# Optimization experiments

Hardware: AMD Instinct MI355X
Metric: run time of the kernel (lower is better)

The kernel has to match this reference:

```python
import jax, jax.numpy as jnp
import numpy as np

DIM = 768
NUM_HEADS = 12
HEAD_DIM = DIM // NUM_HEADS
SCALE = HEAD_DIM ** -0.5
NEG = -9e15


def setup_inputs() -> dict:
    key = jax.random.key(0)
    ks = jax.random.split(key, 8)
    B, N, M, C = 4, 1024, 2048, DIM
    q = jax.random.normal(ks[0], (B, N, C), dtype=jnp.float32)
    kv = jax.random.normal(ks[1], (B, M, C), dtype=jnp.float32)
    mask = jax.random.randint(ks[2], (B, 1, N, M), 0, 2, dtype=jnp.int32)
    s = 1.0 / np.sqrt(C)
    Wq = jax.random.normal(ks[3], (C, C), dtype=jnp.float32) * s      # nn.Linear(dim, dim), no bias
    Wkv = jax.random.normal(ks[4], (2 * C, C), dtype=jnp.float32) * s  # nn.Linear(dim, 2*dim), no bias
    Wproj = jax.random.normal(ks[5], (C, C), dtype=jnp.float32) * s
    bproj = jax.random.normal(ks[6], (C,), dtype=jnp.float32) * s
    return {"q": q, "kv": kv, "Wq": Wq, "Wkv": Wkv, "Wproj": Wproj, "bproj": bproj, "mask": mask}


def reference(q, kv, Wq, Wkv, Wproj, bproj, mask):
    B, M, C = kv.shape
    _, N, _ = q.shape
    H, d = NUM_HEADS, HEAD_DIM
    # kv projection -> [B, M, 2, H, d] -> k, v: [B, H, M, d]
    kvp = (kv @ Wkv.T).reshape(B, M, 2, H, d)
    k = kvp[:, :, 0].transpose(0, 2, 1, 3)
    v = kvp[:, :, 1].transpose(0, 2, 1, 3)
    # q projection -> [B, H, N, d], pre-scaled
    qp = (q @ Wq.T).reshape(B, N, H, d).transpose(0, 2, 1, 3) * SCALE
    attn = jnp.einsum('bhnd,bhmd->bhnm', qp, k)  # [B, H, N, M]
    attn = jnp.where(mask == 0, NEG, attn)
    attn = jax.nn.softmax(attn, axis=-1)
    # attn_drop / proj_drop have rate 0.0 (eval): identity
    x = jnp.einsum('bhnm,bhmd->bhnd', attn, v)
    x = x.transpose(0, 2, 1, 3).reshape(B, N, C)
    x = x @ Wproj.T + bproj
    return x
```

## Files before the change

### kernel.cpp

```cpp
#include <hip/hip_runtime.h>
#include <hip/hip_bf16.h>


typedef short    s16x8  __attribute__((ext_vector_type(8)));
typedef short    s16x4  __attribute__((ext_vector_type(4)));
typedef float    f32x4  __attribute__((ext_vector_type(4)));
typedef _Float16 f16x8  __attribute__((ext_vector_type(8)));
typedef _Float16 f16x4  __attribute__((ext_vector_type(4)));
typedef _Float16 f16x2  __attribute__((ext_vector_type(2)));

#define NUM_H 12
#define DIM   768
#define NQ    1024
#define MK    2048
#define QK_SCALE_LOG2E 0.18033688f

__device__ __forceinline__ short f2h(float v) {
    _Float16 h = (_Float16)v;
    return __builtin_bit_cast(short, h);
}
__device__ __forceinline__ float h2f(short v) {
    return (float)__builtin_bit_cast(_Float16, v);
}
__device__ __forceinline__ f32x4 mfma16x32(f16x8 a, f16x8 b, f32x4 c) {
    return __builtin_amdgcn_mfma_f32_16x16x32_f16(a, b, c, 0, 0, 0);
}
__device__ __forceinline__ f16x2 pk2h(float a, float b) {
    return __builtin_bit_cast(f16x2, __builtin_amdgcn_cvt_pkrtz(a, b));
}

__global__ __launch_bounds__(256) void prep_kernel(
    const float* __restrict__ q, const float* __restrict__ kv,
    const float* __restrict__ Wq, const float* __restrict__ Wkv,
    const float* __restrict__ Wp, const int* __restrict__ mask,
    short* __restrict__ q_h, short* __restrict__ kv_h,
    short* __restrict__ Wq_h, short* __restrict__ Wkv_h,
    short* __restrict__ Wp_h, unsigned char* __restrict__ mbytes)
{
    int bid = blockIdx.x;
    if (bid < 5760) {
        const float* s; short* d; long base;
        if (bid < 1536)      { s = q;   d = q_h;   base = (long)bid * 2048; }
        else if (bid < 4608) { s = kv;  d = kv_h;  base = (long)(bid - 1536) * 2048; }
        else if (bid < 4896) { s = Wq;  d = Wq_h;  base = (long)(bid - 4608) * 2048; }
        else if (bid < 5472) { s = Wkv; d = Wkv_h; base = (long)(bid - 4896) * 2048; }
        else                 { s = Wp;  d = Wp_h;  base = (long)(bid - 5472) * 2048; }
        long i = base + threadIdx.x * 8;
        float4 a = *(const float4*)(s + i);
        float4 b = *(const float4*)(s + i + 4);
        s16x8 r;
        r[0] = f2h(a.x); r[1] = f2h(a.y); r[2] = f2h(a.z); r[3] = f2h(a.w);
        r[4] = f2h(b.x); r[5] = f2h(b.y); r[6] = f2h(b.z); r[7] = f2h(b.w);
        *(s16x8*)(d + i) = r;
    } else {
        long base = (long)(bid - 5760) * 2048 + threadIdx.x * 8;
        int4 m0 = *(const int4*)(mask + base);
        int4 m1 = *(const int4*)(mask + base + 4);
        unsigned v = (unsigned)(m0.x != 0)        | ((unsigned)(m0.y != 0) << 1)
                   | ((unsigned)(m0.z != 0) << 2) | ((unsigned)(m0.w != 0) << 3)
                   | ((unsigned)(m1.x != 0) << 4) | ((unsigned)(m1.y != 0) << 5)
                   | ((unsigned)(m1.z != 0) << 6) | ((unsigned)(m1.w << 7) & 0x80);
        v = (v & 0x7f) | ((unsigned)(m1.w != 0) << 7);
        mbytes[base >> 3] = (unsigned char)v;
    }
}

__device__ __forceinline__ void gemm_core(
    short* smem,
    const short* __restrict__ A, const short* __restrict__ Bt,
    int Ncols, int mode, const float* __restrict__ bias,
    short* __restrict__ outb, short* __restrict__ outb2,
    float* __restrict__ outf, int bid)
{
    short (*As)[72] = (short(*)[72])smem;
    short (*Bs)[72] = (short(*)[72])(smem + 9216);

    int ntiles = Ncols >> 7;
    int m0 = (bid / ntiles) << 7;
    int n0 = (bid % ntiles) << 7;
    int t = threadIdx.x;
    int w = t >> 6, lane = t & 63, quad = lane >> 4, l16 = lane & 15;
    int wm = (w & 1) << 6, wn = (w >> 1) << 6;

    f32x4 zero4 = {0.f, 0.f, 0.f, 0.f};
    f32x4 acc[4][4];
    for (int i = 0; i < 4; i++)
        for (int j = 0; j < 4; j++) acc[i][j] = zero4;

    int lr = t >> 1;
    int lc = (t & 1) << 5;
    const short* Ap = A + (long)(m0 + lr) * DIM + lc;
    const short* Bp = Bt + (long)(n0 + lr) * DIM + lc;

    s16x8 a0[4], b0[4], a1[4], b1[4];
    #pragma unroll
    for (int c = 0; c < 4; c++) {
        a0[c] = *(const s16x8*)(Ap + c * 8);
        b0[c] = *(const s16x8*)(Bp + c * 8);
        a1[c] = *(const s16x8*)(Ap + 64 + c * 8);
        b1[c] = *(const s16x8*)(Bp + 64 + c * 8);
    }

    auto mfma_tile = [&]() {
        #pragma unroll
        for (int kh = 0; kh < 2; kh++) {
            f16x8 af[4], bfr[4];
            #pragma unroll
            for (int i = 0; i < 4; i++)
                af[i] = __builtin_bit_cast(f16x8,
                    *(const s16x8*)&As[wm + i * 16 + l16][kh * 32 + quad * 8]);
            #pragma unroll
            for (int j = 0; j < 4; j++)
                bfr[j] = __builtin_bit_cast(f16x8,
                    *(const s16x8*)&Bs[wn + j * 16 + l16][kh * 32 + quad * 8]);
            #pragma unroll
            for (int i = 0; i < 4; i++)
                #pragma unroll
                for (int j = 0; j < 4; j++)
                    acc[i][j] = mfma16x32(af[i], bfr[j], acc[i][j]);
        }
    };

    for (int kt = 0; kt < DIM; kt += 128) {
        __syncthreads();
        #pragma unroll
        for (int c = 0; c < 4; c++) {
            *(s16x8*)&As[lr][lc + c * 8] = a0[c];
            *(s16x8*)&Bs[lr][lc + c * 8] = b0[c];
        }
        __syncthreads();
        if (kt + 128 < DIM) {
            #pragma unroll
            for (int c = 0; c < 4; c++) {
                a0[c] = *(const s16x8*)(Ap + kt + 128 + c * 8);
                b0[c] = *(const s16x8*)(Bp + kt + 128 + c * 8);
            }
        }
        mfma_tile();
        __syncthreads();
        #pragma unroll
        for (int c = 0; c < 4; c++) {
            *(s16x8*)&As[lr][lc + c * 8] = a1[c];
            *(s16x8*)&Bs[lr][lc + c * 8] = b1[c];
        }
        __syncthreads();
        if (kt + 192 < DIM) {
            #pragma unroll
            for (int c = 0; c < 4; c++) {
                a1[c] = *(const s16x8*)(Ap + kt + 192 + c * 8);
                b1[c] = *(const s16x8*)(Bp + kt + 192 + c * 8);
            }
        }
        mfma_tile();
    }

    __syncthreads();

    if (mode == 2) {
        #pragma unroll
        for (int i = 0; i < 4; i++)
            #pragma unroll
            for (int j = 0; j < 4; j++)
                #pragma unroll
                for (int r = 0; r < 4; r++) {
                    int row = m0 + wm + i * 16 + quad * 4 + r;
                    int col = n0 + wn + j * 16 + l16;
                    outf[(long)row * DIM + col] = acc[i][j][r] + bias[col];
                }
        return;
    }

    short (*Cs)[136] = (short(*)[136])smem;
    bool vreg = (mode == 1) && (n0 >= DIM);

    if (!vreg) {
        float sc = (mode == 0) ? QK_SCALE_LOG2E : 1.0f;
        #pragma unroll
        for (int i = 0; i < 4; i++)
            #pragma unroll
            for (int j = 0; j < 4; j++)
                #pragma unroll
                for (int r = 0; r < 4; r++)
                    Cs[wm + i * 16 + quad * 4 + r][wn + j * 16 + l16] =
                        f2h(acc[i][j][r] * sc);
    } else {
        #pragma unroll
        for (int i = 0; i < 4; i++)
            #pragma unroll
            for (int j = 0; j < 4; j++) {
                int c = wn + j * 16 + l16;
                int r0 = wm + i * 16 + quad * 4;
                s16x4 pk;
                pk[0] = f2h(acc[i][j][0]); pk[1] = f2h(acc[i][j][1]);
                pk[2] = f2h(acc[i][j][2]); pk[3] = f2h(acc[i][j][3]);
                *(s16x4*)&Cs[c][r0] = pk;
            }
    }
    __syncthreads();

    if (!vreg) {
        int hb2 = n0 >> 6;
        long rowsN = (mode == 0) ? NQ : MK;
        int b = (int)(m0 / rowsN);
        int rb = (int)(m0 % rowsN);
        short* ob0 = outb + ((long)(b * NUM_H + hb2) * rowsN + rb) * 64;
        short* ob1 = outb + ((long)(b * NUM_H + hb2 + 1) * rowsN + rb) * 64;
        #pragma unroll
        for (int k2 = 0; k2 < 8; k2++) {
            int ch = k2 * 256 + t;
            int half = ch >> 10, off = ch & 1023;
            s16x8 vd = *(const s16x8*)&Cs[off >> 3][(half << 6) + ((off & 7) << 3)];
            *(s16x8*)((half ? ob1 : ob0) + off * 8) = vd;
        }
    } else {
        int hb2 = (n0 - DIM) >> 6;
        int b = m0 >> 11, rb = m0 & 2047;
        #pragma unroll
        for (int k2 = 0; k2 < 8; k2++) {
            int ch = k2 * 256 + t;
            int c = ch >> 4, woff = (ch & 15) << 3;
            s16x8 vd = *(const s16x8*)&Cs[c][woff];
            int half = c >> 6, dd = c & 63;
            *(s16x8*)(outb2 + (((long)(b * NUM_H + hb2 + half) * 64 + dd) * MK + rb) + woff) = vd;
        }
    }
}

__global__ __launch_bounds__(256) void gemm12_kernel(
    const short* __restrict__ qh, const short* __restrict__ Wqh,
    const short* __restrict__ kvh, const short* __restrict__ Wkvh,
    short* __restrict__ qp, short* __restrict__ kk, short* __restrict__ vt)
{
    __shared__ short smem[18432];
    if (blockIdx.x < 192)
        gemm_core(smem, qh, Wqh, 768, 0, nullptr, qp, nullptr, nullptr, blockIdx.x);
    else
        gemm_core(smem, kvh, Wkvh, 1536, 1, nullptr, kk, vt, nullptr, blockIdx.x - 192);
}

__global__ __launch_bounds__(256) void gemm3_kernel(
    const short* __restrict__ xb, const short* __restrict__ Wph,
    const float* __restrict__ bias, float* __restrict__ out)
{
    __shared__ short smem[18432];
    gemm_core(smem, xb, Wph, 768, 2, bias, nullptr, nullptr, out, blockIdx.x);
}

__global__ __launch_bounds__(256) void attn_kernel(
    const short* __restrict__ qp, const short* __restrict__ kk,
    const short* __restrict__ vt, const unsigned* __restrict__ mb,
    short* __restrict__ po, float* __restrict__ pl)
{
    __shared__ short qs[128][72];
    __shared__ short ks[64][72];
    __shared__ short vs[64][72];

    int bid = blockIdx.x;
    int bh = bid % 48;
    int rest = bid / 48;
    int mhalf = rest & 1, nt = rest >> 1;
    int h = bh % NUM_H, b = bh / NUM_H;
    int n0 = nt << 7;
    int t = threadIdx.x, w = t >> 6, lane = t & 63, quad = lane >> 4, l16 = lane & 15;

    const short* qbase = qp + ((long)bh * NQ + n0) * 64;
    const short* kbase = kk + (long)bh * MK * 64 + (long)mhalf * 1024 * 64;
    const short* vbase = vt + (long)bh * 64 * MK + mhalf * 1024;
    const unsigned* mrow0 = mb + ((long)b * NQ + n0 + (w << 5) + l16) * 64 + (mhalf << 5);
    const unsigned* mrow1 = mrow0 + 16 * 64;

    {
        int qr = t >> 1, c0q = (t & 1) << 5;
        #pragma unroll
        for (int c = 0; c < 4; c++)
            *(s16x8*)&qs[qr][c0q + c * 8] = *(const s16x8*)(qbase + qr * 64 + c0q + c * 8);
    }
    __syncthreads();
    f16x8 bq[2][2];
    #pragma unroll
    for (int s2 = 0; s2 < 2; s2++)
        #pragma unroll
        for (int kh = 0; kh < 2; kh++)
            bq[s2][kh] = __builtin_bit_cast(f16x8,
                *(const s16x8*)&qs[(w << 5) + (s2 << 4) + l16][kh * 32 + quad * 8]);

    int sr = t >> 2, c0 = (t & 3) << 4;
    int pr = (sr & 32) + ((sr & 4) << 2) + ((sr & 24) >> 1) + (sr & 3);
    const short* kp = kbase + (long)sr * 64 + c0;
    const short* vp = vbase + (long)sr * MK + c0;

    s16x8 k0 = *(const s16x8*)(kp);
    s16x8 k1 = *(const s16x8*)(kp + 8);
    s16x8 v0 = *(const s16x8*)(vp);
    s16x8 v1 = *(const s16x8*)(vp + 8);
    uint2 mwv0 = *(const uint2*)(mrow0);
    uint2 mwv1 = *(const uint2*)(mrow1);

    f32x4 zero4 = {0.f, 0.f, 0.f, 0.f};
    f32x4 o[2][4], ol[2];
    #pragma unroll
    for (int s2 = 0; s2 < 2; s2++) {
        ol[s2] = zero4;
        for (int j = 0; j < 4; j++) o[s2][j] = zero4;
    }
    const f16x8 ones = {(_Float16)1.f, (_Float16)1.f, (_Float16)1.f, (_Float16)1.f,
                        (_Float16)1.f, (_Float16)1.f, (_Float16)1.f, (_Float16)1.f};

    for (int mt = 0; mt < 1024; mt += 64) {
        __syncthreads();
        *(s16x8*)&ks[pr][c0]     = k0;
        *(s16x8*)&ks[pr][c0 + 8] = k1;
        *(s16x8*)&vs[sr][c0]     = v0;
        *(s16x8*)&vs[sr][c0 + 8] = v1;
        unsigned cm[2][2] = {{mwv0.x, mwv0.y}, {mwv1.x, mwv1.y}};
        __syncthreads();
        if (mt + 64 < 1024) {
            k0 = *(const s16x8*)(kp + (long)(mt + 64) * 64);
            k1 = *(const s16x8*)(kp + (long)(mt + 64) * 64 + 8);
            v0 = *(const s16x8*)(vp + mt + 64);
            v1 = *(const s16x8*)(vp + mt + 64 + 8);
            mwv0 = *(const uint2*)(mrow0 + ((mt + 64) >> 5));
            mwv1 = *(const uint2*)(mrow1 + ((mt + 64) >> 5));
        }

        f32x4 s[2][4];
        #pragma unroll
        for (int jj = 0; jj < 4; jj++) { s[0][jj] = zero4; s[1][jj] = zero4; }
        #pragma unroll
        for (int kh = 0; kh < 2; kh++)
            #pragma unroll
            for (int jj = 0; jj < 4; jj++) {
                f16x8 ak = __builtin_bit_cast(f16x8,
                    *(const s16x8*)&ks[jj * 16 + l16][kh * 32 + quad * 8]);
                s[0][jj] = mfma16x32(ak, bq[0][kh], s[0][jj]);
                s[1][jj] = mfma16x32(ak, bq[1][kh], s[1][jj]);
            }

        f16x8 pa[2][2];
        #pragma unroll
        for (int s2 = 0; s2 < 2; s2++)
            #pragma unroll
            for (int j2 = 0; j2 < 2; j2++) {
                unsigned wsel = cm[s2][j2];
                f16x2 pk[4];
                #pragma unroll
                for (int sub = 0; sub < 2; sub++) {
                    unsigned bits = wsel >> ((quad << 3) + (sub << 2));
                    const f32x4& sv = s[s2][j2 * 2 + sub];
                    float p0 = (bits & 1u)        ? __builtin_amdgcn_exp2f(sv[0]) : 0.f;
                    float p1 = ((bits >> 1) & 1u) ? __builtin_amdgcn_exp2f(sv[1]) : 0.f;
                    float p2 = ((bits >> 2) & 1u) ? __builtin_amdgcn_exp2f(sv[2]) : 0.f;
                    float p3 = ((bits >> 3) & 1u) ? __builtin_amdgcn_exp2f(sv[3]) : 0.f;
                    pk[sub * 2]     = pk2h(p0, p1);
                    pk[sub * 2 + 1] = pk2h(p2, p3);
                }
                f16x4 lo = __builtin_shufflevector(pk[0], pk[1], 0, 1, 2, 3);
                f16x4 hi = __builtin_shufflevector(pk[2], pk[3], 0, 1, 2, 3);
                pa[s2][j2] = __builtin_shufflevector(lo, hi, 0, 1, 2, 3, 4, 5, 6, 7);
            }

        #pragma unroll
        for (int j2 = 0; j2 < 2; j2++) {
            ol[0] = mfma16x32(pa[0][j2], ones, ol[0]);
            ol[1] = mfma16x32(pa[1][j2], ones, ol[1]);
            #pragma unroll
            for (int jd = 0; jd < 4; jd++) {
                f16x8 bv = __builtin_bit_cast(f16x8,
                    *(const s16x8*)&vs[jd * 16 + l16][j2 * 32 + quad * 8]);
                o[0][jd] = mfma16x32(pa[0][j2], bv, o[0][jd]);
                o[1][jd] = mfma16x32(pa[1][j2], bv, o[1][jd]);
            }
        }
    }

    long slot = (long)(mhalf * 384 + bh * 8 + nt);
    __syncthreads();
    #pragma unroll
    for (int s2 = 0; s2 < 2; s2++) {
        #pragma unroll
        for (int jd = 0; jd < 4; jd++)
            #pragma unroll
            for (int rr = 0; rr < 4; rr++)
                qs[(w << 5) + (s2 << 4) + quad * 4 + rr][jd * 16 + l16] =
                    f2h(o[s2][jd][rr]);
        if (l16 == 0) {
            #pragma unroll
            for (int rr = 0; rr < 4; rr++)
                pl[slot * 128 + (w << 5) + (s2 << 4) + quad * 4 + rr] = ol[s2][rr];
        }
    }
    __syncthreads();
    short* pbase = po + slot * 128 * 64;
    #pragma unroll
    for (int k2 = 0; k2 < 4; k2++) {
        int ch = k2 * 256 + t;
        int row = ch >> 3, cc = (ch & 7) << 3;
        *(s16x8*)(pbase + row * 64 + cc) = *(const s16x8*)&qs[row][cc];
    }
}

__global__ __launch_bounds__(256) void combine_kernel(
    const short* __restrict__ po, const float* __restrict__ pl,
    short* __restrict__ xb)
{
    int g = blockIdx.x * 256 + threadIdx.x;
    int rs = g >> 3, c8 = (g & 7) << 3;
    int bh = rs >> 10, rem = rs & 1023;
    int nt = rem >> 7, r = rem & 127;
    int b = bh / NUM_H, h = bh % NUM_H;
    int n = (nt << 7) + r;

    float l = pl[rs] + pl[49152 + rs];
    float linv = 1.0f / l;
    s16x8 x0 = *(const s16x8*)(po + (long)rs * 64 + c8);
    s16x8 x1 = *(const s16x8*)(po + (long)(49152 + rs) * 64 + c8);
    s16x8 r8;
    #pragma unroll
    for (int i = 0; i < 8; i++)
        r8[i] = f2h((h2f(x0[i]) + h2f(x1[i])) * linv);
    *(s16x8*)(xb + ((long)(b * NQ) + n) * DIM + h * 64 + c8) = r8;
}

extern "C" void kernel_launch(void* const* d_in, const int* in_sizes, int n_in,
                              void* d_out, int out_size, void* d_ws, size_t ws_size,
                              hipStream_t stream)
{
    const float* q     = (const float*)d_in[0];
    const float* kv    = (const float*)d_in[1];
    const float* Wq    = (const float*)d_in[2];
    const float* Wkv   = (const float*)d_in[3];
    const float* Wproj = (const float*)d_in[4];
    const float* bproj = (const float*)d_in[5];
    const int*   mask  = (const int*)d_in[6];
    float* out = (float*)d_out;

    char* ws = (char*)d_ws;
    short* q_h   = (short*)ws; ws += (size_t)4096 * 768 * 2;
    short* kv_h  = (short*)ws; ws += (size_t)8192 * 768 * 2;
    short* Wq_h  = (short*)ws; ws += (size_t)768 * 768 * 2;
    short* Wkv_h = (short*)ws; ws += (size_t)1536 * 768 * 2;
    short* Wp_h  = (short*)ws; ws += (size_t)768 * 768 * 2;
    short* qp    = (short*)ws; ws += (size_t)4096 * 768 * 2;
    short* kk    = (short*)ws; ws += (size_t)8192 * 768 * 2;
    short* vt    = (short*)ws; ws += (size_t)8192 * 768 * 2;
    short* xb    = (short*)ws; ws += (size_t)4096 * 768 * 2;
    unsigned char* mbytes = (unsigned char*)ws; ws += (size_t)1 << 20;
    short* po    = (short*)ws; ws += (size_t)2 * 49152 * 64 * 2;
    float* pl    = (float*)ws;

    prep_kernel<<<9856, 256, 0, stream>>>(q, kv, Wq, Wkv, Wproj, mask,
                                          q_h, kv_h, Wq_h, Wkv_h, Wp_h, mbytes);
    gemm12_kernel<<<960, 256, 0, stream>>>(q_h, Wq_h, kv_h, Wkv_h, qp, kk, vt);
    attn_kernel<<<768, 256, 0, stream>>>(qp, kk, vt, (const unsigned*)mbytes, po, pl);
    combine_kernel<<<1536, 256, 0, stream>>>(po, pl, xb);
    gemm3_kernel<<<192, 256, 0, stream>>>(xb, Wp_h, bproj, out);
}
```

Before: 214.9 us.

## Load K fragments directly from global into registers, bypassing shared memory

The attention kernel no longer stages K tiles through LDS. Each wave now loads its own permuted K MFMA operand fragments straight from global memory into registers, and the next tile's K loads are issued after the QK MFMAs. This removes the LDS writes and reads for K and shrinks shared memory use. In exchange, each of the four waves reloads the same K tile from global/L2 (four times the K traffic), needs more registers, and has to wait out global latency instead of LDS latency. A small cleanup of the mask-packing expression is also included.

```diff
diff --git a/kernel.cpp b/kernel.cpp
--- a/kernel.cpp
+++ b/kernel.cpp
@@ -59,8 +59,7 @@
         unsigned v = (unsigned)(m0.x != 0)        | ((unsigned)(m0.y != 0) << 1)
                    | ((unsigned)(m0.z != 0) << 2) | ((unsigned)(m0.w != 0) << 3)
                    | ((unsigned)(m1.x != 0) << 4) | ((unsigned)(m1.y != 0) << 5)
-                   | ((unsigned)(m1.z != 0) << 6) | ((unsigned)(m1.w << 7) & 0x80);
-        v = (v & 0x7f) | ((unsigned)(m1.w != 0) << 7);
+                   | ((unsigned)(m1.z != 0) << 6) | ((unsigned)(m1.w != 0) << 7);
         mbytes[base >> 3] = (unsigned char)v;
     }
 }
@@ -252,7 +251,6 @@
     short* __restrict__ po, float* __restrict__ pl)
 {
     __shared__ short qs[128][72];
-    __shared__ short ks[64][72];
     __shared__ short vs[64][72];
 
     int bid = blockIdx.x;
@@ -284,13 +282,23 @@
             bq[s2][kh] = __builtin_bit_cast(f16x8,
                 *(const s16x8*)&qs[(w << 5) + (s2 << 4) + l16][kh * 32 + quad * 8]);
 
+    const short* kfp[4];
+    #pragma unroll
+    for (int jj = 0; jj < 4; jj++) {
+        int p = jj * 16 + l16;
+        int row = (p & 32) + ((p & 12) << 1) + ((p & 16) >> 2) + (p & 3);
+        kfp[jj] = kbase + (long)row * 64 + quad * 8;
+    }
+
     int sr = t >> 2, c0 = (t & 3) << 4;
-    int pr = (sr & 32) + ((sr & 4) << 2) + ((sr & 24) >> 1) + (sr & 3);
-    const short* kp = kbase + (long)sr * 64 + c0;
     const short* vp = vbase + (long)sr * MK + c0;
 
-    s16x8 k0 = *(const s16x8*)(kp);
-    s16x8 k1 = *(const s16x8*)(kp + 8);
+    s16x8 kcur[4][2];
+    #pragma unroll
+    for (int jj = 0; jj < 4; jj++)
+        #pragma unroll
+        for (int kh = 0; kh < 2; kh++)
+            kcur[jj][kh] = *(const s16x8*)(kfp[jj] + kh * 32);
     s16x8 v0 = *(const s16x8*)(vp);
     s16x8 v1 = *(const s16x8*)(vp + 8);
     uint2 mwv0 = *(const uint2*)(mrow0);
@@ -308,33 +316,35 @@
 
     for (int mt = 0; mt < 1024; mt += 64) {
         __syncthreads();
-        *(s16x8*)&ks[pr][c0]     = k0;
-        *(s16x8*)&ks[pr][c0 + 8] = k1;
         *(s16x8*)&vs[sr][c0]     = v0;
         *(s16x8*)&vs[sr][c0 + 8] = v1;
         unsigned cm[2][2] = {{mwv0.x, mwv0.y}, {mwv1.x, mwv1.y}};
         __syncthreads();
+
+        f32x4 s[2][4];
+        #pragma unroll
+        for (int jj = 0; jj < 4; jj++) { s[0][jj] = zero4; s[1][jj] = zero4; }
+        #pragma unroll
+        for (int kh = 0; kh < 2; kh++)
+            #pragma unroll
+            for (int jj = 0; jj < 4; jj++) {
+                f16x8 ak = __builtin_bit_cast(f16x8, kcur[jj][kh]);
+                s[0][jj] = mfma16x32(ak, bq[0][kh], s[0][jj]);
+                s[1][jj] = mfma16x32(ak, bq[1][kh], s[1][jj]);
+            }
+
         if (mt + 64 < 1024) {
-            k0 = *(const s16x8*)(kp + (long)(mt + 64) * 64);
-            k1 = *(const s16x8*)(kp + (long)(mt + 64) * 64 + 8);
+            long koff = (long)(mt + 64) * 64;
+            #pragma unroll
+            for (int jj = 0; jj < 4; jj++)
+                #pragma unroll
+                for (int kh = 0; kh < 2; kh++)
+                    kcur[jj][kh] = *(const s16x8*)(kfp[jj] + koff + kh * 32);
             v0 = *(const s16x8*)(vp + mt + 64);
             v1 = *(const s16x8*)(vp + mt + 64 + 8);
             mwv0 = *(const uint2*)(mrow0 + ((mt + 64) >> 5));
             mwv1 = *(const uint2*)(mrow1 + ((mt + 64) >> 5));
         }
-
-        f32x4 s[2][4];
-        #pragma unroll
-        for (int jj = 0; jj < 4; jj++) { s[0][jj] = zero4; s[1][jj] = zero4; }
-        #pragma unroll
-        for (int kh = 0; kh < 2; kh++)
-            #pragma unroll
-            for (int jj = 0; jj < 4; jj++) {
-                f16x8 ak = __builtin_bit_cast(f16x8,
-                    *(const s16x8*)&ks[jj * 16 + l16][kh * 32 + quad * 8]);
-                s[0][jj] = mfma16x32(ak, bq[0][kh], s[0][jj]);
-                s[1][jj] = mfma16x32(ak, bq[1][kh], s[1][jj]);
-            }
 
         f16x8 pa[2][2];
         #pragma unroll
```

Result: slower. 241.4 us (+12.3%).
